# Kernel optimization log

Hardware: AMD Instinct MI355X
Metric: run time of the kernel (lower is better)

Reference implementation:

```python
import jax, jax.numpy as jnp
import numpy as np

HEADS = 16
D_K = 64  # hidden_units // heads


def setup_inputs() -> dict:
    key = jax.random.key(0)
    ks = jax.random.split(key, 9)
    B, S, D, H = 4, 2048, 1024, 1024  # batch, seq, in_shape, hidden_units
    inputs = jax.random.normal(ks[0], (B, S, D), dtype=jnp.float32)
    # xavier_normal for weights, default bias init ~ small uniform (use zeros for simplicity of baseline? keep uniform like torch)
    def xavier(k, fan_in, fan_out):
        std = jnp.sqrt(2.0 / (fan_in + fan_out))
        return jax.random.normal(k, (fan_out, fan_in), dtype=jnp.float32) * std
    Wq = xavier(ks[1], D, H)
    Wk = xavier(ks[2], D, H)
    Wv = xavier(ks[3], D, H)
    Wo = xavier(ks[4], H, H)
    bound = 1.0 / jnp.sqrt(D)
    bq = jax.random.uniform(ks[5], (H,), minval=-bound, maxval=bound, dtype=jnp.float32)
    bk = jax.random.uniform(ks[6], (H,), minval=-bound, maxval=bound, dtype=jnp.float32)
    bv = jax.random.uniform(ks[7], (H,), minval=-bound, maxval=bound, dtype=jnp.float32)
    bo = jax.random.uniform(ks[8], (H,), minval=-1.0 / jnp.sqrt(H), maxval=1.0 / jnp.sqrt(H), dtype=jnp.float32)
    return {"inputs": inputs, "Wq": Wq, "bq": bq, "Wk": Wk, "bk": bk,
            "Wv": Wv, "bv": bv, "Wo": Wo, "bo": bo}


def reference(inputs, Wq, bq, Wk, bk, Wv, bv, Wo, bo):
    B, S, _ = inputs.shape
    # QKV projections -> (B, S, heads, d_k)
    def proj(W, b):
        return (inputs @ W.T + b).reshape(B, S, HEADS, D_K)
    q = proj(Wq, bq)
    k = proj(Wk, bk)
    v = proj(Wv, bv)
    scale = 1.0 / jnp.sqrt(jnp.float32(D_K))
    # scores: (B, heads, S, S)
    scores = jnp.einsum('bqhd,bkhd->bhqk', q, k) * scale
    attn = jax.nn.softmax(scores, axis=-1)
    # (B, heads, S, d_k) -> (B, S, heads*d_k)
    ctx = jnp.einsum('bhqk,bkhd->bqhd', attn, v).reshape(B, S, HEADS * D_K)
    out = ctx @ Wo.T + bo
    return out
```

## Files before the change

### kernel.cpp

```cpp
#include <hip/hip_runtime.h>
#include <stdint.h>


using bf16x8 = __attribute__((ext_vector_type(8))) short;
using f32x4  = __attribute__((ext_vector_type(4))) float;

#define QSCALE 0.18033688f

__device__ __forceinline__ unsigned short f2bf(float f) {
    unsigned u = __builtin_bit_cast(unsigned, f);
    u += 0x7fffu + ((u >> 16) & 1u);
    return (unsigned short)(u >> 16);
}

__device__ __forceinline__ void gld16(const void* g, void* l) {
    void* gnc = (void*)g;
    __builtin_amdgcn_global_load_lds((__attribute__((address_space(1))) void*)gnc,
                                     (__attribute__((address_space(3))) void*)l,
                                     16, 0, 0);
}

__device__ __forceinline__ int swz(int R, int g) {
    return R * 64 + ((g ^ (R & 7)) << 3);
}

__global__ void castall(const float* __restrict__ X, const float* __restrict__ Wq,
                        const float* __restrict__ Wk, const float* __restrict__ Wv,
                        const float* __restrict__ Wo, unsigned short* __restrict__ Xb,
                        unsigned short* __restrict__ Wqkvb, unsigned short* __restrict__ Wob) {
    const int bx = blockIdx.x;
    const float* src; unsigned short* dst; int idx;
    if (bx < 8192) { src = X; dst = Xb; idx = bx * 256 + threadIdx.x; }
    else {
        const int r = bx - 8192, w = r >> 10;
        idx = (r & 1023) * 256 + threadIdx.x;
        src = (w == 0) ? Wq : (w == 1) ? Wk : (w == 2) ? Wv : Wo;
        dst = (w == 3) ? Wob : Wqkvb + (size_t)w * 1048576;
    }
    float4 v = ((const float4*)src)[idx];
    ((ushort4*)dst)[idx] = make_ushort4(f2bf(v.x), f2bf(v.y), f2bf(v.z), f2bf(v.w));
}

__global__ __launch_bounds__(256) void gemm_qkv(const unsigned short* __restrict__ A,
                                                const unsigned short* __restrict__ Wqkv,
                                                const float* __restrict__ bq,
                                                const float* __restrict__ bk,
                                                const float* __restrict__ bv,
                                                unsigned short* __restrict__ Qb,
                                                unsigned short* __restrict__ Kb,
                                                unsigned short* __restrict__ Vt) {
    __shared__ alignas(16) unsigned short sA[128 * 64];
    __shared__ alignas(16) unsigned short sB[128 * 64];
    const int tid  = threadIdx.x;
    const int lane = tid & 63;
    const int wave = tid >> 6;
    const int quad = lane >> 4;
    const int l15  = lane & 15;
    const int lr   = lane >> 3;
    const int lcs  = (((lane & 7) ^ lr) << 3);
    const int nb   = blockIdx.x >> 3;
    const int col0 = (blockIdx.x & 7) * 128;
    const int row0 = blockIdx.y * 128;
    const unsigned short* W = Wqkv + ((size_t)nb << 20);
    const float* bias = (nb == 0) ? bq : (nb == 1) ? bk : bv;
    const int wm = wave >> 1, wn = wave & 1;

    f32x4 acc[4][4];
#pragma unroll
    for (int i = 0; i < 4; i++)
#pragma unroll
        for (int j = 0; j < 4; j++) acc[i][j] = f32x4{0.f, 0.f, 0.f, 0.f};

    for (int kt = 0; kt < 16; ++kt) {
        const int k0 = kt * 64;
#pragma unroll
        for (int i = 0; i < 4; i++) {
            const int c = wave * 4 + i;
            const int r = c * 8 + lr;
            gld16(A + (size_t)(row0 + r) * 1024 + k0 + lcs, &sA[c * 512]);
            gld16(W + (size_t)(col0 + r) * 1024 + k0 + lcs, &sB[c * 512]);
        }
        __syncthreads();
#pragma unroll
        for (int kx = 0; kx < 2; ++kx) {
            bf16x8 a[4], b[4];
#pragma unroll
            for (int i = 0; i < 4; i++) {
                a[i] = *(const bf16x8*)&sA[swz(wm * 64 + i * 16 + l15, kx * 4 + quad)];
                b[i] = *(const bf16x8*)&sB[swz(wn * 64 + i * 16 + l15, kx * 4 + quad)];
            }
#pragma unroll
            for (int i = 0; i < 4; i++)
#pragma unroll
                for (int j = 0; j < 4; j++)
                    acc[i][j] = __builtin_amdgcn_mfma_f32_16x16x32_bf16(a[i], b[j], acc[i][j], 0, 0, 0);
        }
        __syncthreads();
    }

    const float sc = (nb == 0) ? QSCALE : 1.0f;
#pragma unroll
    for (int i = 0; i < 4; i++) {
#pragma unroll
        for (int j = 0; j < 4; j++) {
            const int col   = col0 + wn * 64 + j * 16 + l15;
            const float bvv = bias[col];
            const int rbase = row0 + wm * 64 + i * 16 + quad * 4;
            if (nb == 2) {
                const int bb = rbase >> 11;
                const int s  = rbase & 2047;
                unsigned short* dst = Vt + ((size_t)(bb * 1024 + col)) * 2048 + s;
                *(ushort4*)dst = make_ushort4(f2bf(acc[i][j][0] + bvv), f2bf(acc[i][j][1] + bvv),
                                              f2bf(acc[i][j][2] + bvv), f2bf(acc[i][j][3] + bvv));
            } else {
                unsigned short* C = (nb == 0) ? Qb : Kb;
#pragma unroll
                for (int r = 0; r < 4; r++)
                    C[(size_t)(rbase + r) * 1024 + col] = f2bf((acc[i][j][r] + bvv) * sc);
            }
        }
    }
}

__global__ __launch_bounds__(256) void gemm_out(const unsigned short* __restrict__ A,
                                                const unsigned short* __restrict__ W,
                                                const float* __restrict__ bias,
                                                float* __restrict__ C) {
    __shared__ alignas(16) unsigned short sA[128 * 64];
    __shared__ alignas(16) unsigned short sB[128 * 64];
    const int tid  = threadIdx.x;
    const int lane = tid & 63;
    const int wave = tid >> 6;
    const int quad = lane >> 4;
    const int l15  = lane & 15;
    const int lr   = lane >> 3;
    const int lcs  = (((lane & 7) ^ lr) << 3);
    const int row0 = blockIdx.y * 128;
    const int col0 = blockIdx.x * 128;
    const int wm = wave >> 1, wn = wave & 1;

    f32x4 acc[4][4];
#pragma unroll
    for (int i = 0; i < 4; i++)
#pragma unroll
        for (int j = 0; j < 4; j++) acc[i][j] = f32x4{0.f, 0.f, 0.f, 0.f};

    for (int kt = 0; kt < 16; ++kt) {
        const int k0 = kt * 64;
#pragma unroll
        for (int i = 0; i < 4; i++) {
            const int c = wave * 4 + i;
            const int r = c * 8 + lr;
            gld16(A + (size_t)(row0 + r) * 1024 + k0 + lcs, &sA[c * 512]);
            gld16(W + (size_t)(col0 + r) * 1024 + k0 + lcs, &sB[c * 512]);
        }
        __syncthreads();
#pragma unroll
        for (int kx = 0; kx < 2; ++kx) {
            bf16x8 a[4], b[4];
#pragma unroll
            for (int i = 0; i < 4; i++) {
                a[i] = *(const bf16x8*)&sA[swz(wm * 64 + i * 16 + l15, kx * 4 + quad)];
                b[i] = *(const bf16x8*)&sB[swz(wn * 64 + i * 16 + l15, kx * 4 + quad)];
            }
#pragma unroll
            for (int i = 0; i < 4; i++)
#pragma unroll
                for (int j = 0; j < 4; j++)
                    acc[i][j] = __builtin_amdgcn_mfma_f32_16x16x32_bf16(a[i], b[j], acc[i][j], 0, 0, 0);
        }
        __syncthreads();
    }

#pragma unroll
    for (int i = 0; i < 4; i++) {
#pragma unroll
        for (int j = 0; j < 4; j++) {
            const int col   = col0 + wn * 64 + j * 16 + l15;
            const float bvv = bias[col];
            const int rbase = row0 + wm * 64 + i * 16 + quad * 4;
#pragma unroll
            for (int r = 0; r < 4; r++)
                C[(size_t)(rbase + r) * 1024 + col] = acc[i][j][r] + bvv;
        }
    }
}

__global__ __launch_bounds__(256) void attn(const unsigned short* __restrict__ Q,
                                            const unsigned short* __restrict__ K,
                                            const unsigned short* __restrict__ Vt,
                                            unsigned short* __restrict__ Ctx) {
    __shared__ alignas(16) unsigned short Kl[64 * 64];
    __shared__ alignas(16) unsigned short Vl[64 * 64];
    __shared__ alignas(16) unsigned short Pl[4][32][72];

    const int tid  = threadIdx.x;
    const int lane = tid & 63;
    const int wave = tid >> 6;
    const int quad = lane >> 4;
    const int l15  = lane & 15;
    const int lr   = lane >> 3;
    const int lcs  = (((lane & 7) ^ lr) << 3);

    const int qt = blockIdx.x, h = blockIdx.y, b = blockIdx.z;
    const int q0 = qt * 128;
    const size_t tokbase = (size_t)b * 2048;

    bf16x8 qa[2][2];
#pragma unroll
    for (int mt = 0; mt < 2; ++mt)
#pragma unroll
        for (int kx = 0; kx < 2; ++kx)
            qa[mt][kx] = *(const bf16x8*)(Q + (tokbase + q0 + wave * 32 + mt * 16 + l15) * 1024 +
                                          h * 64 + kx * 32 + quad * 8);

    f32x4 O[2][4];
#pragma unroll
    for (int mt = 0; mt < 2; ++mt)
#pragma unroll
        for (int nt = 0; nt < 4; ++nt) O[mt][nt] = f32x4{0.f, 0.f, 0.f, 0.f};
    float rs[2] = {0.f, 0.f};

    for (int kt = 0; kt < 32; ++kt) {
#pragma unroll
        for (int i = 0; i < 2; i++) {
            const int c  = wave * 2 + i;
            const int rr = c * 8 + lr;
            gld16(K + (tokbase + kt * 64 + rr) * 1024 + h * 64 + lcs, &Kl[c * 512]);
            gld16(Vt + ((size_t)(b * 1024 + h * 64 + rr)) * 2048 + kt * 64 + lcs, &Vl[c * 512]);
        }
        __syncthreads();

        f32x4 St[4][2];
#pragma unroll
        for (int nt = 0; nt < 4; ++nt)
#pragma unroll
            for (int mt = 0; mt < 2; ++mt) St[nt][mt] = f32x4{0.f, 0.f, 0.f, 0.f};
#pragma unroll
        for (int kx = 0; kx < 2; ++kx) {
            bf16x8 kb[4];
#pragma unroll
            for (int nt = 0; nt < 4; ++nt)
                kb[nt] = *(const bf16x8*)&Kl[swz(nt * 16 + l15, kx * 4 + quad)];
#pragma unroll
            for (int nt = 0; nt < 4; ++nt)
#pragma unroll
                for (int mt = 0; mt < 2; ++mt)
                    St[nt][mt] = __builtin_amdgcn_mfma_f32_16x16x32_bf16(kb[nt], qa[mt][kx], St[nt][mt], 0, 0, 0);
        }

#pragma unroll
        for (int mt = 0; mt < 2; ++mt) {
            float rsl = 0.f;
#pragma unroll
            for (int nt = 0; nt < 4; ++nt) {
                float p0 = exp2f(St[nt][mt][0]);
                float p1 = exp2f(St[nt][mt][1]);
                float p2 = exp2f(St[nt][mt][2]);
                float p3 = exp2f(St[nt][mt][3]);
                rsl += (p0 + p1) + (p2 + p3);
                *(ushort4*)&Pl[wave][mt * 16 + l15][nt * 16 + quad * 4] =
                    make_ushort4(f2bf(p0), f2bf(p1), f2bf(p2), f2bf(p3));
            }
            rs[mt] += rsl;
        }

#pragma unroll
        for (int kx = 0; kx < 2; ++kx) {
            bf16x8 pa[2], vb[4];
#pragma unroll
            for (int mt = 0; mt < 2; ++mt)
                pa[mt] = *(const bf16x8*)&Pl[wave][mt * 16 + l15][kx * 32 + quad * 8];
#pragma unroll
            for (int nt = 0; nt < 4; ++nt)
                vb[nt] = *(const bf16x8*)&Vl[swz(nt * 16 + l15, kx * 4 + quad)];
#pragma unroll
            for (int mt = 0; mt < 2; ++mt)
#pragma unroll
                for (int nt = 0; nt < 4; ++nt)
                    O[mt][nt] = __builtin_amdgcn_mfma_f32_16x16x32_bf16(pa[mt], vb[nt], O[mt][nt], 0, 0, 0);
        }
        __syncthreads();
    }

    float linv[2][4];
#pragma unroll
    for (int mt = 0; mt < 2; ++mt) {
        float lv = rs[mt];
        lv += __shfl_xor(lv, 16);
        lv += __shfl_xor(lv, 32);
#pragma unroll
        for (int r = 0; r < 4; ++r)
            linv[mt][r] = 1.0f / __shfl(lv, quad * 4 + r);
    }

#pragma unroll
    for (int mt = 0; mt < 2; ++mt) {
#pragma unroll
        for (int r = 0; r < 4; ++r) {
            const int row   = q0 + wave * 32 + mt * 16 + quad * 4 + r;
            const size_t base = (tokbase + row) * 1024 + h * 64;
#pragma unroll
            for (int nt = 0; nt < 4; ++nt)
                Ctx[base + nt * 16 + l15] = f2bf(O[mt][nt][r] * linv[mt][r]);
        }
    }
}

extern "C" void kernel_launch(void* const* d_in, const int* in_sizes, int n_in,
                              void* d_out, int out_size, void* d_ws, size_t ws_size,
                              hipStream_t stream) {
    (void)in_sizes; (void)n_in; (void)out_size; (void)ws_size;
    const float* X  = (const float*)d_in[0];
    const float* Wq = (const float*)d_in[1];
    const float* bq = (const float*)d_in[2];
    const float* Wk = (const float*)d_in[3];
    const float* bk = (const float*)d_in[4];
    const float* Wv = (const float*)d_in[5];
    const float* bv = (const float*)d_in[6];
    const float* Wo = (const float*)d_in[7];
    const float* bo = (const float*)d_in[8];

    char* ws = (char*)d_ws;
    unsigned short* Xb    = (unsigned short*)(ws);
    unsigned short* Qb    = (unsigned short*)(ws + (size_t)16 * 1048576);
    unsigned short* Kb    = (unsigned short*)(ws + (size_t)32 * 1048576);
    unsigned short* Vt    = (unsigned short*)(ws + (size_t)48 * 1048576);
    unsigned short* Wqkvb = (unsigned short*)(ws + (size_t)64 * 1048576);
    unsigned short* Wob   = (unsigned short*)(ws + (size_t)70 * 1048576);
    unsigned short* Ctx   = Xb;

    castall<<<dim3(12288), 256, 0, stream>>>(X, Wq, Wk, Wv, Wo, Xb, Wqkvb, Wob);
    gemm_qkv<<<dim3(24, 64), 256, 0, stream>>>(Xb, Wqkvb, bq, bk, bv, Qb, Kb, Vt);
    attn<<<dim3(16, 16, 4), 256, 0, stream>>>(Qb, Kb, Vt, Ctx);
    gemm_out<<<dim3(8, 64), 256, 0, stream>>>(Ctx, Wob, bo, (float*)d_out);
}
```

Before: 329.8 us.

## Stage QKV GEMM epilogue through LDS for coalesced stores and use cheaper bf16 packing

The QKV projection epilogue now writes bias-added bf16 tiles into shared memory, transposed for V, and then writes them to global memory as contiguous 16-byte rows instead of scattered 2-byte or 8-byte stores. The bf16 conversion is replaced with a round-half-up add plus a byte permute that packs two values per instruction. The attention softmax uses the raw hardware exp2 intrinsic in place of exp2f. This trades an extra LDS round trip and barrier for coalesced writes, and the new rounding differs slightly from round-to-nearest-even.

```diff
diff --git a/kernel.cpp b/kernel.cpp
--- a/kernel.cpp
+++ b/kernel.cpp
@@ -11,6 +11,12 @@
     unsigned u = __builtin_bit_cast(unsigned, f);
     u += 0x7fffu + ((u >> 16) & 1u);
     return (unsigned short)(u >> 16);
+}
+
+__device__ __forceinline__ unsigned pack2bf(float f0, float f1) {
+    unsigned u0 = __builtin_bit_cast(unsigned, f0) + 0x8000u;
+    unsigned u1 = __builtin_bit_cast(unsigned, f1) + 0x8000u;
+    return __builtin_amdgcn_perm(u1, u0, 0x07060302);
 }
 
 __device__ __forceinline__ void gld16(const void* g, void* l) {
@@ -38,7 +44,7 @@
         dst = (w == 3) ? Wob : Wqkvb + (size_t)w * 1048576;
     }
     float4 v = ((const float4*)src)[idx];
-    ((ushort4*)dst)[idx] = make_ushort4(f2bf(v.x), f2bf(v.y), f2bf(v.z), f2bf(v.w));
+    ((uint2*)dst)[idx] = make_uint2(pack2bf(v.x, v.y), pack2bf(v.z, v.w));
 }
 
 __global__ __launch_bounds__(256) void gemm_qkv(const unsigned short* __restrict__ A,
@@ -49,8 +55,11 @@
                                                 unsigned short* __restrict__ Qb,
                                                 unsigned short* __restrict__ Kb,
                                                 unsigned short* __restrict__ Vt) {
-    __shared__ alignas(16) unsigned short sA[128 * 64];
-    __shared__ alignas(16) unsigned short sB[128 * 64];
+    __shared__ alignas(16) unsigned short smem[17408];
+    unsigned short* sA = smem;
+    unsigned short* sB = smem + 8192;
+    unsigned short* OT = smem;
+
     const int tid  = threadIdx.x;
     const int lane = tid & 63;
     const int wave = tid >> 6;
@@ -98,27 +107,50 @@
         __syncthreads();
     }
 
-    const float sc = (nb == 0) ? QSCALE : 1.0f;
-#pragma unroll
-    for (int i = 0; i < 4; i++) {
-#pragma unroll
-        for (int j = 0; j < 4; j++) {
-            const int col   = col0 + wn * 64 + j * 16 + l15;
-            const float bvv = bias[col];
-            const int rbase = row0 + wm * 64 + i * 16 + quad * 4;
-            if (nb == 2) {
-                const int bb = rbase >> 11;
-                const int s  = rbase & 2047;
-                unsigned short* dst = Vt + ((size_t)(bb * 1024 + col)) * 2048 + s;
-                *(ushort4*)dst = make_ushort4(f2bf(acc[i][j][0] + bvv), f2bf(acc[i][j][1] + bvv),
-                                              f2bf(acc[i][j][2] + bvv), f2bf(acc[i][j][3] + bvv));
-            } else {
-                unsigned short* C = (nb == 0) ? Qb : Kb;
+    if (nb != 2) {
+        const float sc = (nb == 0) ? QSCALE : 1.0f;
+#pragma unroll
+        for (int i = 0; i < 4; i++) {
+#pragma unroll
+            for (int j = 0; j < 4; j++) {
+                const int ct  = wn * 64 + j * 16 + l15;
+                const float bvv = bias[col0 + ct];
+                const int rt  = wm * 64 + i * 16 + quad * 4;
 #pragma unroll
                 for (int r = 0; r < 4; r++)
-                    C[(size_t)(rbase + r) * 1024 + col] = f2bf((acc[i][j][r] + bvv) * sc);
-            }
-        }
+                    OT[(rt + r) * 136 + ct] = f2bf((acc[i][j][r] + bvv) * sc);
+            }
+        }
+    } else {
+#pragma unroll
+        for (int i = 0; i < 4; i++) {
+#pragma unroll
+            for (int j = 0; j < 4; j++) {
+                const int ct  = wn * 64 + j * 16 + l15;
+                const float bvv = bias[col0 + ct];
+                const int rt  = wm * 64 + i * 16 + quad * 4;
+                *(uint2*)&OT[ct * 136 + rt] =
+                    make_uint2(pack2bf(acc[i][j][0] + bvv, acc[i][j][1] + bvv),
+                               pack2bf(acc[i][j][2] + bvv, acc[i][j][3] + bvv));
+            }
+        }
+    }
+    __syncthreads();
+
+    const int rr   = wave * 32 + (lane >> 1);
+    const int half = lane & 1;
+    if (nb != 2) {
+        unsigned short* C = (nb == 0) ? Qb : Kb;
+        unsigned short* gdst = C + (size_t)(row0 + rr) * 1024 + col0 + half * 64;
+#pragma unroll
+        for (int k = 0; k < 8; k++)
+            *(bf16x8*)(gdst + k * 8) = *(const bf16x8*)&OT[rr * 136 + half * 64 + k * 8];
+    } else {
+        const int bb = row0 >> 11, s0l = row0 & 2047;
+        unsigned short* gdst = Vt + ((size_t)(bb * 1024 + col0 + rr)) * 2048 + s0l + half * 64;
+#pragma unroll
+        for (int k = 0; k < 8; k++)
+            *(bf16x8*)(gdst + k * 8) = *(const bf16x8*)&OT[rr * 136 + half * 64 + k * 8];
     }
 }
 
@@ -254,13 +286,13 @@
             float rsl = 0.f;
 #pragma unroll
             for (int nt = 0; nt < 4; ++nt) {
-                float p0 = exp2f(St[nt][mt][0]);
-                float p1 = exp2f(St[nt][mt][1]);
-                float p2 = exp2f(St[nt][mt][2]);
-                float p3 = exp2f(St[nt][mt][3]);
+                float p0 = __builtin_amdgcn_exp2f(St[nt][mt][0]);
+                float p1 = __builtin_amdgcn_exp2f(St[nt][mt][1]);
+                float p2 = __builtin_amdgcn_exp2f(St[nt][mt][2]);
+                float p3 = __builtin_amdgcn_exp2f(St[nt][mt][3]);
                 rsl += (p0 + p1) + (p2 + p3);
-                *(ushort4*)&Pl[wave][mt * 16 + l15][nt * 16 + quad * 4] =
-                    make_ushort4(f2bf(p0), f2bf(p1), f2bf(p2), f2bf(p3));
+                *(uint2*)&Pl[wave][mt * 16 + l15][nt * 16 + quad * 4] =
+                    make_uint2(pack2bf(p0, p1), pack2bf(p2, p3));
             }
             rs[mt] += rsl;
         }
```

Measured after the change: 302.8 us. 1.09x faster.
